# Kernel optimization log

Hardware: AMD Instinct MI355X
Metric: run time of the kernel (lower is better)

The kernel has to match this reference:

```python
import jax, jax.numpy as jnp
import numpy as np

B, S, D = 2, 2048, 1024
H = 16
HD = D // H  # 64
FORESIGHT = -1e9  # masked_fill value for non-causal positions


def setup_inputs() -> dict:
    key = jax.random.key(0)
    ks = jax.random.split(key, 8)
    s = 0.02
    return {
        "x": jax.random.normal(ks[0], (B, S, D), dtype=jnp.float32),
        "Wq": jax.random.normal(ks[1], (D, H * HD), dtype=jnp.float32) * s,
        "bq": jax.random.normal(ks[2], (H * HD,), dtype=jnp.float32) * s,
        "Wk": jax.random.normal(ks[3], (D, H * HD), dtype=jnp.float32) * s,
        "Wv": jax.random.normal(ks[4], (D, H * HD), dtype=jnp.float32) * s,
        "Wo": jax.random.normal(ks[5], (H * HD, D), dtype=jnp.float32) * s,
        "bo": jax.random.normal(ks[6], (D,), dtype=jnp.float32) * s,
    }


def reference(x, Wq, bq, Wk, Wv, Wo, bo):
    b, s, _ = x.shape
    # projections -> [B, H, S, HD]
    q = (x @ Wq + bq).reshape(b, s, H, HD).transpose(0, 2, 1, 3)
    k = (x @ Wk).reshape(b, s, H, HD).transpose(0, 2, 1, 3)
    v = (x @ Wv).reshape(b, s, H, HD).transpose(0, 2, 1, 3)
    # scores [B, H, S, S]
    scores = jnp.einsum("bhqd,bhkd->bhqk", q, k) / jnp.sqrt(jnp.float32(HD))
    # ALiBi bias: slope_h * j (key position), broadcast over queries
    slopes = 2.0 ** (-8.0 * jnp.arange(1, H + 1, dtype=jnp.float32) / H)
    positions = jnp.arange(s, dtype=jnp.float32)
    scores = scores - slopes[None, :, None, None] * positions[None, None, None, :]
    # causal mask: fill strictly-upper triangle with foresight
    causal = jnp.tril(jnp.ones((s, s), dtype=bool))
    scores = jnp.where(causal[None, None, :, :], scores, FORESIGHT)
    attn = jax.nn.softmax(scores, axis=-1)
    out = jnp.einsum("bhqk,bhkd->bhqd", attn, v)
    out = out.transpose(0, 2, 1, 3).reshape(b, s, H * HD)
    return out @ Wo + bo
```

## Files before the change

kernel.cpp:

```cpp
#include <hip/hip_runtime.h>
#include <stdint.h>

#define DDIM 1024
#define HH 16
#define HDIM 64
#define SS 2048

typedef short bf16x8 __attribute__((ext_vector_type(8)));
typedef short bf16x4 __attribute__((ext_vector_type(4)));
typedef float f32x4 __attribute__((ext_vector_type(4)));
typedef unsigned short u16;

__device__ __forceinline__ unsigned f2bf(float f) {
  unsigned u = __builtin_bit_cast(unsigned, f);
  u = u + 0x7FFFu + ((u >> 16) & 1u);
  return u >> 16;
}

__device__ __forceinline__ void mfma16(f32x4& c, bf16x4 a, bf16x4 b) {
  asm("v_mfma_f32_16x16x16_bf16 %0, %1, %2, %0" : "+v"(c) : "v"(a), "v"(b));
}

__device__ __forceinline__ void gload16(const void* g, void* l) {
  __builtin_amdgcn_global_load_lds(
      (const __attribute__((address_space(1))) unsigned int*)g,
      (__attribute__((address_space(3))) unsigned int*)l, 16, 0, 0);
}

__global__ void k_convert_x(const float* __restrict__ x, u16* __restrict__ xb) {
  int i = (blockIdx.x * 256 + threadIdx.x) * 4;
  float4 v = *(const float4*)(x + i);
  ushort4 o;
  o.x = (u16)f2bf(v.x); o.y = (u16)f2bf(v.y); o.z = (u16)f2bf(v.z); o.w = (u16)f2bf(v.w);
  *(ushort4*)(xb + i) = o;
}

__global__ void k_transpose_w(const float* __restrict__ w0, const float* __restrict__ w1,
                              const float* __restrict__ w2, const float* __restrict__ w3,
                              u16* __restrict__ wt) {
  __shared__ float t[64][65];
  int z = blockIdx.z;
  const float* src = (z == 0) ? w0 : (z == 1) ? w1 : (z == 2) ? w2 : w3;
  u16* dst = wt + (size_t)z * DDIM * DDIM;
  int k0 = blockIdx.x * 64, n0 = blockIdx.y * 64;
  int tid = threadIdx.x;
  int c4 = tid & 15, rr = tid >> 4;
  for (int rep = 0; rep < 4; rep++) {
    int r = rr + rep * 16;
    float4 v = *(const float4*)(src + (size_t)(k0 + r) * DDIM + n0 + c4 * 4);
    t[r][c4 * 4 + 0] = v.x; t[r][c4 * 4 + 1] = v.y;
    t[r][c4 * 4 + 2] = v.z; t[r][c4 * 4 + 3] = v.w;
  }
  __syncthreads();
  for (int rep = 0; rep < 4; rep++) {
    int n = rr + rep * 16;
    ushort4 o;
    o.x = (u16)f2bf(t[c4 * 4 + 0][n]); o.y = (u16)f2bf(t[c4 * 4 + 1][n]);
    o.z = (u16)f2bf(t[c4 * 4 + 2][n]); o.w = (u16)f2bf(t[c4 * 4 + 3][n]);
    *(ushort4*)(dst + (size_t)(n0 + n) * DDIM + k0 + c4 * 4) = o;
  }
}

template <int MODE>
__global__ __launch_bounds__(256, 2) void k_gemm(const u16* __restrict__ A,
                                                 const u16* __restrict__ BT,
                                                 const float* __restrict__ bias,
                                                 void* __restrict__ O0,
                                                 void* __restrict__ O1,
                                                 void* __restrict__ O2) {
  __shared__ __align__(16) u16 lA[128 * 64];
  __shared__ __align__(16) u16 lB[128 * 64];
  const int tid = threadIdx.x;
  const int l = tid & 63, w = tid >> 6;
  const int wm = w >> 1, wn = w & 1;
  const int m0 = blockIdx.x * 128, n0 = blockIdx.y * 128;
  const int lr = l >> 4, lc = l & 15;

  const int srow = l >> 3;
  const int scol = ((l & 7) ^ srow) * 8;

  f32x4 acc[4][4];
  for (int mi = 0; mi < 4; mi++)
    for (int ni = 0; ni < 4; ni++)
      acc[mi][ni] = f32x4{0.f, 0.f, 0.f, 0.f};

  for (int kk = 0; kk < 16; kk++) {
    const int k0 = kk * 64;
    for (int i = 0; i < 4; i++) {
      int c = w * 4 + i;
      gload16(A + (size_t)(m0 + c * 8 + srow) * DDIM + k0 + scol, (char*)lA + c * 1024);
      gload16(BT + (size_t)(n0 + c * 8 + srow) * DDIM + k0 + scol, (char*)lB + c * 1024);
    }
    __syncthreads();
    for (int ks = 0; ks < 2; ks++) {
      bf16x8 af[4], bfr[4];
      for (int mi = 0; mi < 4; mi++) {
        int row = wm * 64 + mi * 16 + lc;
        int slot = (ks * 4 + lr) ^ (row & 7);
        af[mi] = *(const bf16x8*)((const char*)lA + row * 128 + slot * 16);
      }
      for (int ni = 0; ni < 4; ni++) {
        int row = wn * 64 + ni * 16 + lc;
        int slot = (ks * 4 + lr) ^ (row & 7);
        bfr[ni] = *(const bf16x8*)((const char*)lB + row * 128 + slot * 16);
      }
      for (int mi = 0; mi < 4; mi++)
        for (int ni = 0; ni < 4; ni++)
          acc[mi][ni] = __builtin_amdgcn_mfma_f32_16x16x32_bf16(af[mi], bfr[ni], acc[mi][ni], 0, 0, 0);
    }
    __syncthreads();
  }

  if (MODE == 0) {
    const int which = blockIdx.y >> 3;
    if (which == 0) {
      u16* C = (u16*)O0;
      for (int mi = 0; mi < 4; mi++)
        for (int ni = 0; ni < 4; ni++) {
          int nl = (n0 + wn * 64 + ni * 16 + lc) & 1023;
          float badd = bias[nl];
          for (int r = 0; r < 4; r++) {
            int m = m0 + wm * 64 + mi * 16 + lr * 4 + r;
            C[(size_t)m * DDIM + nl] = (u16)f2bf(acc[mi][ni][r] + badd);
          }
        }
    } else if (which == 1) {
      u16* C = (u16*)O1;
      for (int mi = 0; mi < 4; mi++)
        for (int ni = 0; ni < 4; ni++) {
          int nl = (n0 + wn * 64 + ni * 16 + lc) & 1023;
          for (int r = 0; r < 4; r++) {
            int m = m0 + wm * 64 + mi * 16 + lr * 4 + r;
            C[(size_t)m * DDIM + nl] = (u16)f2bf(acc[mi][ni][r]);
          }
        }
    } else {
      u16* C = (u16*)O2;
      for (int mi = 0; mi < 4; mi++)
        for (int ni = 0; ni < 4; ni++) {
          int nl = (n0 + wn * 64 + ni * 16 + lc) & 1023;
          int h = nl >> 6, hd = nl & 63;
          int m = m0 + wm * 64 + mi * 16 + lr * 4;
          int b = m >> 11, s = m & 2047;
          unsigned d0 = f2bf(acc[mi][ni][0]) | (f2bf(acc[mi][ni][1]) << 16);
          unsigned d1 = f2bf(acc[mi][ni][2]) | (f2bf(acc[mi][ni][3]) << 16);
          u16* p = C + ((size_t)((b * HH + h) * HDIM + hd)) * SS + s;
          *(unsigned*)(p) = d0;
          *(unsigned*)(p + 2) = d1;
        }
    }
  } else {
    float* C = (float*)O0;
    for (int mi = 0; mi < 4; mi++)
      for (int ni = 0; ni < 4; ni++) {
        int n = n0 + wn * 64 + ni * 16 + lc;
        float badd = bias[n];
        for (int r = 0; r < 4; r++) {
          int m = m0 + wm * 64 + mi * 16 + lr * 4 + r;
          C[(size_t)m * DDIM + n] = acc[mi][ni][r] + badd;
        }
      }
  }
}

__device__ __forceinline__ void attn_tile(int kt, bool masked, int kfhi,
                                          const char* lKc, const char* lVc,
                                          const bf16x8 qf[2], f32x4 of[4],
                                          float& mrun, float& lrun,
                                          float slope, int lr, int lc, int q_glob) {
  f32x4 sf[8];
#pragma unroll
  for (int kf = 0; kf < 8; kf++) sf[kf] = f32x4{0.f, 0.f, 0.f, 0.f};
#pragma unroll
  for (int ks = 0; ks < 2; ks++)
#pragma unroll
    for (int kf = 0; kf < 8; kf++) {
      if (kf >= kfhi) continue;
      int key = kf * 16 + lc;
      int slot = (ks * 4 + lr) ^ (lc & 7);
      bf16x8 a = *(const bf16x8*)(lKc + key * 128 + slot * 16);
      sf[kf] = __builtin_amdgcn_mfma_f32_16x16x32_bf16(a, qf[ks], sf[kf], 0, 0, 0);
    }

  float tmax = -INFINITY;
#pragma unroll
  for (int kf = 0; kf < 8; kf++) {
    if (kf >= kfhi) continue;
#pragma unroll
    for (int r = 0; r < 4; r++) {
      int key = kt * 128 + kf * 16 + lr * 4 + r;
      float sv = sf[kf][r] * 0.125f - slope * (float)key;
      if (masked && key > q_glob) sv = -1e9f;
      sf[kf][r] = sv;
      tmax = fmaxf(tmax, sv);
    }
  }
  tmax = fmaxf(tmax, __shfl_xor(tmax, 16));
  tmax = fmaxf(tmax, __shfl_xor(tmax, 32));

  if (tmax > mrun) {
    float corr = __expf(mrun - tmax);
    lrun *= corr;
#pragma unroll
    for (int mf = 0; mf < 4; mf++) {
      of[mf][0] *= corr; of[mf][1] *= corr; of[mf][2] *= corr; of[mf][3] *= corr;
    }
    mrun = tmax;
  }

  f32x4 ps = f32x4{0.f, 0.f, 0.f, 0.f};
  bf16x4 pb[8];
#pragma unroll
  for (int kf = 0; kf < 8; kf++) {
    if (kf >= kfhi) continue;
    unsigned a0 = f2bf(__expf(sf[kf][0] - mrun));
    unsigned a1 = f2bf(__expf(sf[kf][1] - mrun));
    unsigned a2 = f2bf(__expf(sf[kf][2] - mrun));
    unsigned a3 = f2bf(__expf(sf[kf][3] - mrun));
    uint2 uu;
    uu.x = a0 | (a1 << 16);
    uu.y = a2 | (a3 << 16);
    pb[kf] = __builtin_bit_cast(bf16x4, uu);
    ps[0] += __builtin_bit_cast(float, a0 << 16);
    ps[1] += __builtin_bit_cast(float, a1 << 16);
    ps[2] += __builtin_bit_cast(float, a2 << 16);
    ps[3] += __builtin_bit_cast(float, a3 << 16);
  }
  float psum = (ps[0] + ps[1]) + (ps[2] + ps[3]);
  psum += __shfl_xor(psum, 16);
  psum += __shfl_xor(psum, 32);
  lrun += psum;

#pragma unroll
  for (int kf = 0; kf < 8; kf++) {
    if (kf >= kfhi) continue;
    int g2 = (kf << 1) + (lr >> 1);
#pragma unroll
    for (int mf = 0; mf < 4; mf++) {
      int hd = mf * 16 + lc;
      int byte = hd * 256 + ((g2 ^ (hd & 7)) << 4) + ((lr & 1) << 3);
      bf16x4 va = *(const bf16x4*)(lVc + byte);
      mfma16(of[mf], va, pb[kf]);
    }
  }
}

__global__ __launch_bounds__(256, 4) void k_attn(const u16* __restrict__ Q,
                                                 const u16* __restrict__ Kg,
                                                 const u16* __restrict__ Vt,
                                                 u16* __restrict__ AO) {
  __shared__ __align__(16) u16 lK[128 * 64];
  __shared__ __align__(16) u16 lV[64 * 128];

  const int tid = threadIdx.x;
  const int l = tid & 63, w = tid >> 6;
  const int lr = l >> 4, lc = l & 15;
  const int bh = blockIdx.x;
  const int b = bh >> 4, h = bh & 15;
  const int yq = blockIdx.y;
  const int fk = yq & 7, fj = yq >> 3;
  const int qt = (fj == 0) ? fk : (fj == 1) ? (15 - fk) : (fj == 2) ? (16 + fk) : (31 - fk);

  const float slope = exp2f(-0.5f * (float)(h + 1));
  const int q_glob = qt * 64 + w * 16 + lc;

  bf16x8 qf[2];
#pragma unroll
  for (int ks = 0; ks < 2; ks++)
    qf[ks] = *(const bf16x8*)(Q + (size_t)(b * SS + q_glob) * DDIM + h * HDIM + ks * 32 + lr * 8);

  f32x4 of[4];
#pragma unroll
  for (int mf = 0; mf < 4; mf++) of[mf] = f32x4{0.f, 0.f, 0.f, 0.f};
  float mrun = -INFINITY, lrun = 0.f;

  const int srowK = l >> 3;
  const int scolK = ((l & 7) ^ srowK) * 8;
  const int nkt = qt / 2 + 1;

  auto stage = [&](int kt) {
#pragma unroll
    for (int i = 0; i < 4; i++) {
      int c = w * 4 + i;
      gload16(Kg + (size_t)(b * SS + kt * 128 + c * 8 + srowK) * DDIM + h * HDIM + scolK,
              (char*)lK + c * 1024);
      int hd = c * 4 + lr;
      gload16(Vt + ((size_t)bh * HDIM + hd) * SS + kt * 128 + (((l & 15) ^ (hd & 7)) << 3),
              (char*)lV + c * 1024);
    }
  };

  for (int kt = 0; kt < nkt - 1; kt++) {
    stage(kt);
    __syncthreads();
    attn_tile(kt, false, 8, (const char*)lK, (const char*)lV, qf, of, mrun, lrun,
              slope, lr, lc, q_glob);
    __syncthreads();
  }
  stage(nkt - 1);
  __syncthreads();
  if (qt & 1)
    attn_tile(nkt - 1, true, 8, (const char*)lK, (const char*)lV, qf, of, mrun, lrun,
              slope, lr, lc, q_glob);
  else
    attn_tile(nkt - 1, true, 4, (const char*)lK, (const char*)lV, qf, of, mrun, lrun,
              slope, lr, lc, q_glob);

  float inv = 1.f / lrun;
  u16* obase = AO + (size_t)(b * SS + q_glob) * DDIM + h * HDIM;
#pragma unroll
  for (int mf = 0; mf < 4; mf++) {
    uint2 uu;
    uu.x = f2bf(of[mf][0] * inv) | (f2bf(of[mf][1] * inv) << 16);
    uu.y = f2bf(of[mf][2] * inv) | (f2bf(of[mf][3] * inv) << 16);
    *(uint2*)(obase + mf * 16 + lr * 4) = uu;
  }
}

extern "C" void kernel_launch(void* const* d_in, const int* in_sizes, int n_in,
                              void* d_out, int out_size, void* d_ws, size_t ws_size,
                              hipStream_t stream) {
  const float* x  = (const float*)d_in[0];
  const float* Wq = (const float*)d_in[1];
  const float* bq = (const float*)d_in[2];
  const float* Wk = (const float*)d_in[3];
  const float* Wv = (const float*)d_in[4];
  const float* Wo = (const float*)d_in[5];
  const float* bo = (const float*)d_in[6];
  float* out = (float*)d_out;

  u16* ws = (u16*)d_ws;
  const size_t MEG = 1024 * 1024;
  u16* xb = ws;
  u16* WT = ws + 4 * MEG;
  u16* Qb = ws + 8 * MEG;
  u16* Kb = ws + 12 * MEG;
  u16* Vt = ws + 16 * MEG;
  u16* AO = ws + 20 * MEG;

  k_convert_x<<<dim3(4096), dim3(256), 0, stream>>>(x, xb);
  k_transpose_w<<<dim3(16, 16, 4), dim3(256), 0, stream>>>(Wq, Wk, Wv, Wo, WT);
  k_gemm<0><<<dim3(32, 24), dim3(256), 0, stream>>>(xb, WT, bq, (void*)Qb, (void*)Kb, (void*)Vt);
  k_attn<<<dim3(32, 32), dim3(256), 0, stream>>>(Qb, Kb, Vt, AO);
  k_gemm<1><<<dim3(32, 8), dim3(256), 0, stream>>>(AO, WT + 3 * MEG, bo, (void*)out, nullptr, nullptr);
}
```

Baseline: 123.7 us.

## Double-buffer K/V tiles in attention and route P through LDS for 16x16x32 MFMA

The attention kernel now double-buffers K/V tiles in LDS, prefetching the next tile while computing the current one, and drops one barrier per iteration. Softmax probabilities go through a per-wave LDS scratch buffer, so the PV product uses the wider 16x16x32 bf16 MFMA instead of the 16x16x16 instruction. It also adds s_setprio around MFMA sections, lowers launch bounds occupancy to 2, and flattens the grid to interleave causal query tiles for load balance. The trade-off is roughly double the LDS footprint, extra LDS write/read traffic for P, and possibly lower occupancy.

```diff
diff --git a/kernel.cpp b/kernel.cpp
--- a/kernel.cpp
+++ b/kernel.cpp
@@ -7,7 +7,6 @@
 #define SS 2048
 
 typedef short bf16x8 __attribute__((ext_vector_type(8)));
-typedef short bf16x4 __attribute__((ext_vector_type(4)));
 typedef float f32x4 __attribute__((ext_vector_type(4)));
 typedef unsigned short u16;
 
@@ -15,10 +14,6 @@
   unsigned u = __builtin_bit_cast(unsigned, f);
   u = u + 0x7FFFu + ((u >> 16) & 1u);
   return u >> 16;
-}
-
-__device__ __forceinline__ void mfma16(f32x4& c, bf16x4 a, bf16x4 b) {
-  asm("v_mfma_f32_16x16x16_bf16 %0, %1, %2, %0" : "+v"(c) : "v"(a), "v"(b));
 }
 
 __device__ __forceinline__ void gload16(const void* g, void* l) {
@@ -164,13 +159,14 @@
 }
 
 __device__ __forceinline__ void attn_tile(int kt, bool masked, int kfhi,
-                                          const char* lKc, const char* lVc,
+                                          const char* lKc, const char* lVc, char* lPw,
                                           const bf16x8 qf[2], f32x4 of[4],
                                           float& mrun, float& lrun,
                                           float slope, int lr, int lc, int q_glob) {
   f32x4 sf[8];
 #pragma unroll
   for (int kf = 0; kf < 8; kf++) sf[kf] = f32x4{0.f, 0.f, 0.f, 0.f};
+  __builtin_amdgcn_s_setprio(1);
 #pragma unroll
   for (int ks = 0; ks < 2; ks++)
 #pragma unroll
@@ -181,6 +177,7 @@
       bf16x8 a = *(const bf16x8*)(lKc + key * 128 + slot * 16);
       sf[kf] = __builtin_amdgcn_mfma_f32_16x16x32_bf16(a, qf[ks], sf[kf], 0, 0, 0);
     }
+  __builtin_amdgcn_s_setprio(0);
 
   float tmax = -INFINITY;
 #pragma unroll
@@ -209,57 +206,59 @@
   }
 
   f32x4 ps = f32x4{0.f, 0.f, 0.f, 0.f};
-  bf16x4 pb[8];
 #pragma unroll
   for (int kf = 0; kf < 8; kf++) {
     if (kf >= kfhi) continue;
-    unsigned a0 = f2bf(__expf(sf[kf][0] - mrun));
-    unsigned a1 = f2bf(__expf(sf[kf][1] - mrun));
-    unsigned a2 = f2bf(__expf(sf[kf][2] - mrun));
-    unsigned a3 = f2bf(__expf(sf[kf][3] - mrun));
-    uint2 uu;
-    uu.x = a0 | (a1 << 16);
-    uu.y = a2 | (a3 << 16);
-    pb[kf] = __builtin_bit_cast(bf16x4, uu);
-    ps[0] += __builtin_bit_cast(float, a0 << 16);
-    ps[1] += __builtin_bit_cast(float, a1 << 16);
-    ps[2] += __builtin_bit_cast(float, a2 << 16);
-    ps[3] += __builtin_bit_cast(float, a3 << 16);
+    float p0 = __expf(sf[kf][0] - mrun);
+    float p1 = __expf(sf[kf][1] - mrun);
+    float p2 = __expf(sf[kf][2] - mrun);
+    float p3 = __expf(sf[kf][3] - mrun);
+    ps[0] += p0; ps[1] += p1; ps[2] += p2; ps[3] += p3;
+    int g2 = (kf << 1) + (lr >> 1);
+    char* base = lPw + lc * 256 + ((g2 ^ (lc & 7)) << 4) + ((lr & 1) << 3);
+    *(unsigned*)(base) = f2bf(p0) | (f2bf(p1) << 16);
+    *(unsigned*)(base + 4) = f2bf(p2) | (f2bf(p3) << 16);
   }
   float psum = (ps[0] + ps[1]) + (ps[2] + ps[3]);
   psum += __shfl_xor(psum, 16);
   psum += __shfl_xor(psum, 32);
   lrun += psum;
 
-#pragma unroll
-  for (int kf = 0; kf < 8; kf++) {
-    if (kf >= kfhi) continue;
-    int g2 = (kf << 1) + (lr >> 1);
+  const int kshi = kfhi >> 1;
+  __builtin_amdgcn_s_setprio(1);
+#pragma unroll
+  for (int ks = 0; ks < 4; ks++) {
+    if (ks >= kshi) continue;
+    int slotp = (ks * 4 + lr) ^ (lc & 7);
+    bf16x8 pb = *(const bf16x8*)(lPw + lc * 256 + slotp * 16);
 #pragma unroll
     for (int mf = 0; mf < 4; mf++) {
       int hd = mf * 16 + lc;
-      int byte = hd * 256 + ((g2 ^ (hd & 7)) << 4) + ((lr & 1) << 3);
-      bf16x4 va = *(const bf16x4*)(lVc + byte);
-      mfma16(of[mf], va, pb[kf]);
-    }
-  }
-}
-
-__global__ __launch_bounds__(256, 4) void k_attn(const u16* __restrict__ Q,
+      int slotv = (ks * 4 + lr) ^ (hd & 7);
+      bf16x8 va = *(const bf16x8*)(lVc + hd * 256 + slotv * 16);
+      of[mf] = __builtin_amdgcn_mfma_f32_16x16x32_bf16(va, pb, of[mf], 0, 0, 0);
+    }
+  }
+  __builtin_amdgcn_s_setprio(0);
+}
+
+__global__ __launch_bounds__(256, 2) void k_attn(const u16* __restrict__ Q,
                                                  const u16* __restrict__ Kg,
                                                  const u16* __restrict__ Vt,
                                                  u16* __restrict__ AO) {
-  __shared__ __align__(16) u16 lK[128 * 64];
-  __shared__ __align__(16) u16 lV[64 * 128];
+  __shared__ __align__(16) u16 lK[2][128 * 64];
+  __shared__ __align__(16) u16 lV[2][64 * 128];
+  __shared__ __align__(16) u16 lP[4][16 * 128];
 
   const int tid = threadIdx.x;
   const int l = tid & 63, w = tid >> 6;
   const int lr = l >> 4, lc = l & 15;
-  const int bh = blockIdx.x;
+  const int id = blockIdx.x;
+  const int bh = id & 31;
+  const int s5 = (id >> 5) & 1;
+  const int gg = id >> 6;
+  const int qt = s5 ? (31 - gg) : gg;
   const int b = bh >> 4, h = bh & 15;
-  const int yq = blockIdx.y;
-  const int fk = yq & 7, fj = yq >> 3;
-  const int qt = (fj == 0) ? fk : (fj == 1) ? (15 - fk) : (fj == 2) ? (16 + fk) : (31 - fk);
 
   const float slope = exp2f(-0.5f * (float)(h + 1));
   const int q_glob = qt * 64 + w * 16 + lc;
@@ -277,34 +276,41 @@
   const int srowK = l >> 3;
   const int scolK = ((l & 7) ^ srowK) * 8;
   const int nkt = qt / 2 + 1;
-
-  auto stage = [&](int kt) {
+  char* lPw = (char*)lP[w];
+
+  auto stage = [&](int kt, int bb) {
 #pragma unroll
     for (int i = 0; i < 4; i++) {
       int c = w * 4 + i;
       gload16(Kg + (size_t)(b * SS + kt * 128 + c * 8 + srowK) * DDIM + h * HDIM + scolK,
-              (char*)lK + c * 1024);
+              (char*)lK[bb] + c * 1024);
       int hd = c * 4 + lr;
       gload16(Vt + ((size_t)bh * HDIM + hd) * SS + kt * 128 + (((l & 15) ^ (hd & 7)) << 3),
-              (char*)lV + c * 1024);
+              (char*)lV[bb] + c * 1024);
     }
   };
 
+  stage(0, 0);
+  asm volatile("s_waitcnt vmcnt(0)" ::: "memory");
+  __builtin_amdgcn_s_barrier();
+  asm volatile("" ::: "memory");
+
   for (int kt = 0; kt < nkt - 1; kt++) {
-    stage(kt);
-    __syncthreads();
-    attn_tile(kt, false, 8, (const char*)lK, (const char*)lV, qf, of, mrun, lrun,
-              slope, lr, lc, q_glob);
-    __syncthreads();
-  }
-  stage(nkt - 1);
-  __syncthreads();
+    const int cur = kt & 1;
+    stage(kt + 1, cur ^ 1);
+    attn_tile(kt, false, 8, (const char*)lK[cur], (const char*)lV[cur], lPw,
+              qf, of, mrun, lrun, slope, lr, lc, q_glob);
+    asm volatile("s_waitcnt vmcnt(0)" ::: "memory");
+    __builtin_amdgcn_s_barrier();
+    asm volatile("" ::: "memory");
+  }
+  const int cur = (nkt - 1) & 1;
   if (qt & 1)
-    attn_tile(nkt - 1, true, 8, (const char*)lK, (const char*)lV, qf, of, mrun, lrun,
-              slope, lr, lc, q_glob);
+    attn_tile(nkt - 1, true, 8, (const char*)lK[cur], (const char*)lV[cur], lPw,
+              qf, of, mrun, lrun, slope, lr, lc, q_glob);
   else
-    attn_tile(nkt - 1, true, 4, (const char*)lK, (const char*)lV, qf, of, mrun, lrun,
-              slope, lr, lc, q_glob);
+    attn_tile(nkt - 1, true, 4, (const char*)lK[cur], (const char*)lV[cur], lPw,
+              qf, of, mrun, lrun, slope, lr, lc, q_glob);
 
   float inv = 1.f / lrun;
   u16* obase = AO + (size_t)(b * SS + q_glob) * DDIM + h * HDIM;
@@ -341,6 +347,6 @@
   k_convert_x<<<dim3(4096), dim3(256), 0, stream>>>(x, xb);
   k_transpose_w<<<dim3(16, 16, 4), dim3(256), 0, stream>>>(Wq, Wk, Wv, Wo, WT);
   k_gemm<0><<<dim3(32, 24), dim3(256), 0, stream>>>(xb, WT, bq, (void*)Qb, (void*)Kb, (void*)Vt);
-  k_attn<<<dim3(32, 32), dim3(256), 0, stream>>>(Qb, Kb, Vt, AO);
+  k_attn<<<dim3(1024), dim3(256), 0, stream>>>(Qb, Kb, Vt, AO);
   k_gemm<1><<<dim3(32, 8), dim3(256), 0, stream>>>(AO, WT + 3 * MEG, bo, (void*)out, nullptr, nullptr);
 }
```

After: 121.2 us. 1.02x faster.
